# Kernel optimization log

Measured on AMD Instinct MI355X. Metric: run time of the kernel, lower is better.

Reference implementation:

```python
import jax, jax.numpy as jnp
import numpy as np

N_NODES = 100000
N_EDGES = 1600000
F_IN = 256
HID = 128
N_CLS = 64
K_APPNP = 10
ALPHA = 0.1


def setup_inputs() -> dict:
    key = jax.random.key(0)
    ks = jax.random.split(key, 12)
    x = jax.random.normal(ks[0], (N_NODES, F_IN), dtype=jnp.float32)
    edge_index = jax.random.randint(ks[1], (2, N_EDGES), 0, N_NODES, dtype=jnp.int64)
    def lin(k, fan_in, fan_out):
        s = 1.0 / np.sqrt(fan_in)
        kw, kb = jax.random.split(k)
        W = jax.random.uniform(kw, (fan_in, fan_out), minval=-s, maxval=s, dtype=jnp.float32)
        b = jax.random.uniform(kb, (fan_out,), minval=-s, maxval=s, dtype=jnp.float32)
        return W, b
    W1, b1 = lin(ks[2], F_IN, HID)
    W2, b2 = lin(ks[3], HID, HID)
    Wc, bc = lin(ks[4], HID, N_CLS)
    We, be = lin(ks[5], N_CLS, N_CLS)
    return {"x": x, "edge_index": edge_index, "W1": W1, "b1": b1, "W2": W2,
            "b2": b2, "Wc": Wc, "bc": bc, "We": We, "be": be}


def reference(x, edge_index, W1, b1, W2, b2, Wc, bc, We, be):
    N = x.shape[0]
    loop = jnp.arange(N)
    row = jnp.concatenate([edge_index[0], loop])  # source nodes (+ self loops)
    col = jnp.concatenate([edge_index[1], loop])  # target nodes (+ self loops)
    # symmetric GCN normalization: deg computed on targets
    deg = jax.ops.segment_sum(jnp.ones_like(col, dtype=x.dtype), col, num_segments=N)
    dinv = jnp.where(deg > 0, jax.lax.rsqrt(deg), 0.0)
    norm = dinv[row] * dinv[col]  # [E+N]

    def prop(h):  # normalized scatter-add aggregation
        return jax.ops.segment_sum(h[row] * norm[:, None], col, num_segments=N)

    # GCNConv: transform -> propagate -> bias (dropout is eval no-op)
    h = jax.nn.relu(prop(x @ W1) + b1)
    h = jax.nn.relu(prop(h @ W2) + b2)
    logits = h @ Wc + bc
    ev = jax.nn.relu(logits @ We + be)
    # APPNP: z_{k+1} = (1-alpha) * A_hat z_k + alpha * ev
    z = ev
    for _ in range(K_APPNP):
        z = (1.0 - ALPHA) * prop(z) + ALPHA * ev
    return jax.nn.log_softmax(z, axis=1)
```

## Files before the change

### kernel.cpp

```cpp
#include <hip/hip_runtime.h>
#include <hip/hip_fp16.h>


struct __align__(16) half8 { __half2 h[4]; };
typedef _Float16 f16x8 __attribute__((ext_vector_type(8)));
typedef float f32x4 __attribute__((ext_vector_type(4)));

__global__ __launch_bounds__(256) void k_init(int* deg, int N) {
    int i = blockIdx.x * 256 + threadIdx.x;
    if (i < N) deg[i] = 1;
}

__global__ __launch_bounds__(256) void k_count(const int* __restrict__ dst,
                                               int* deg, int* __restrict__ rank, int E) {
    int e = blockIdx.x * 256 + threadIdx.x;
    if (e < E) {
        int r = atomicAdd(&deg[dst[e]], 1);
        rank[e] = r - 1;
    }
}

__global__ __launch_bounds__(256) void k_scanA(const int* __restrict__ deg, int* bs, int N) {
    __shared__ int s[256];
    int t = threadIdx.x;
    int i = blockIdx.x * 256 + t;
    int c = (i < N) ? (deg[i] - 1) : 0;
    s[t] = c; __syncthreads();
    for (int o = 128; o > 0; o >>= 1) {
        if (t < o) s[t] += s[t + o];
        __syncthreads();
    }
    if (t == 0) bs[blockIdx.x] = s[0];
}

__global__ __launch_bounds__(512) void k_scanB(int* bs, int NB) {
    __shared__ int s[512];
    int t = threadIdx.x;
    int v = (t < NB) ? bs[t] : 0;
    s[t] = v; __syncthreads();
    for (int o = 1; o < 512; o <<= 1) {
        int u = (t >= o) ? s[t - o] : 0;
        __syncthreads();
        s[t] += u;
        __syncthreads();
    }
    if (t < NB) bs[t] = s[t] - v;
}

__global__ __launch_bounds__(256) void k_scanC(const int* __restrict__ deg, const int* __restrict__ bs,
                                               int* row_ptr, float* dinv, int N) {
    __shared__ int s[256];
    int t = threadIdx.x;
    int i = blockIdx.x * 256 + t;
    int c = (i < N) ? (deg[i] - 1) : 0;
    s[t] = c; __syncthreads();
    for (int o = 1; o < 256; o <<= 1) {
        int u = (t >= o) ? s[t - o] : 0;
        __syncthreads();
        s[t] += u;
        __syncthreads();
    }
    if (i < N) {
        int off = bs[blockIdx.x];
        row_ptr[i] = off + s[t] - c;
        dinv[i] = rsqrtf((float)deg[i]);
        if (i == N - 1) row_ptr[N] = off + s[t];
    }
}

__global__ __launch_bounds__(256) void k_fill(const int* __restrict__ src, const int* __restrict__ dst,
                                              const int* __restrict__ row_ptr,
                                              const int* __restrict__ rank,
                                              int* __restrict__ csr_src, int E) {
    int e = blockIdx.x * 256 + threadIdx.x;
    if (e < E) csr_src[row_ptr[dst[e]] + rank[e]] = src[e];
}

__global__ __launch_bounds__(256) void k_fuseW(const float* __restrict__ Wc,
                                               const float* __restrict__ bc,
                                               const float* __restrict__ We,
                                               const float* __restrict__ be,
                                               float* __restrict__ Wf,
                                               float* __restrict__ bf) {
    __shared__ float sWe[64 * 64];
    int tid = threadIdx.x;
    for (int i = tid; i < 64 * 64 / 4; i += 256)
        ((float4*)sWe)[i] = ((const float4*)We)[i];
    __syncthreads();
    for (int idx = tid; idx < 128 * 64; idx += 256) {
        int r = idx >> 6, c = idx & 63;
        float s = 0.f;
#pragma unroll 8
        for (int j = 0; j < 64; j++) s += Wc[r * 64 + j] * sWe[j * 64 + c];
        Wf[idx] = s;
    }
    if (tid < 64) {
        float s = be[tid];
#pragma unroll 8
        for (int j = 0; j < 64; j++) s += bc[j] * sWe[j * 64 + tid];
        bf[tid] = s;
    }
}

__global__ __launch_bounds__(256) void k_prepW(const float* __restrict__ W,
                                               __half* __restrict__ Wt, int K) {
    int idx = blockIdx.x * 256 + threadIdx.x;
    if (idx < 128 * K) {
        int n = idx / K, k = idx % K;
        Wt[idx] = __float2half(W[k * 128 + n]);
    }
}

template <int K, bool IN_F16>
__global__ __launch_bounds__(256) void k_mfma_gemm(const void* __restrict__ Xv,
                                                   const __half* __restrict__ Wt,
                                                   const float* __restrict__ dinv,
                                                   __half* __restrict__ Y, int N) {
    constexpr int PAD = 8;
    constexpr int LDK = K + PAD;
    __shared__ __half sA[32 * LDK];
    int tid = threadIdx.x;
    int rowBase = blockIdx.x * 32;

    if (IN_F16) {
        constexpr int IT = 32 * (K / 8) / 256;
        half8 t[IT];
#pragma unroll
        for (int i = 0; i < IT; i++) {
            int idx = tid + i * 256;
            int r = idx / (K / 8), c8 = idx % (K / 8);
            int rg = rowBase + r; if (rg > N - 1) rg = N - 1;
            t[i] = *(const half8*)&((const __half*)Xv)[(long)rg * K + 8 * c8];
        }
#pragma unroll
        for (int i = 0; i < IT; i++) {
            int idx = tid + i * 256;
            int r = idx / (K / 8), c8 = idx % (K / 8);
            *(half8*)&sA[r * LDK + 8 * c8] = t[i];
        }
    } else {
        constexpr int IT = 32 * (K / 4) / 256;
        float4 t[IT];
#pragma unroll
        for (int i = 0; i < IT; i++) {
            int idx = tid + i * 256;
            int r = idx / (K / 4), c4 = idx % (K / 4);
            int rg = rowBase + r; if (rg > N - 1) rg = N - 1;
            t[i] = *(const float4*)&((const float*)Xv)[(long)rg * K + 4 * c4];
        }
#pragma unroll
        for (int i = 0; i < IT; i++) {
            int idx = tid + i * 256;
            int r = idx / (K / 4), c4 = idx % (K / 4);
            __half2* dst = (__half2*)&sA[r * LDK + 4 * c4];
            dst[0] = __floats2half2_rn(t[i].x, t[i].y);
            dst[1] = __floats2half2_rn(t[i].z, t[i].w);
        }
    }
    __syncthreads();

    int wave = tid >> 6, lane = tid & 63;
    int m = lane & 15, quad = lane >> 4;
    int rw = (wave & 1) * 16;
    int cb = (wave >> 1) * 64;

    f32x4 d[4];
#pragma unroll
    for (int ct = 0; ct < 4; ct++) d[ct] = {0.f, 0.f, 0.f, 0.f};

#pragma unroll
    for (int kh = 0; kh < K / 128; kh++) {
        f16x8 bfr[4][4];
#pragma unroll
        for (int kc = 0; kc < 4; kc++)
#pragma unroll
            for (int ct = 0; ct < 4; ct++)
                bfr[kc][ct] = *(const f16x8*)&Wt[(long)(cb + ct * 16 + m) * K + kh * 128 + kc * 32 + quad * 8];
#pragma unroll
        for (int kc = 0; kc < 4; kc++) {
            const f16x8 a = *(const f16x8*)&sA[(rw + m) * LDK + kh * 128 + kc * 32 + quad * 8];
#pragma unroll
            for (int ct = 0; ct < 4; ct++)
                d[ct] = __builtin_amdgcn_mfma_f32_16x16x32_f16(a, bfr[kc][ct], d[ct], 0, 0, 0);
        }
    }

#pragma unroll
    for (int ct = 0; ct < 4; ct++) {
        int col = cb + ct * 16 + m;
#pragma unroll
        for (int reg = 0; reg < 4; reg++) {
            int row = rowBase + rw + quad * 4 + reg;
            if (row < N)
                Y[(long)row * 128 + col] = __float2half(d[ct][reg] * dinv[row]);
        }
    }
}

__global__ __launch_bounds__(256) void k_cls(const __half* __restrict__ H,
                                             const float* __restrict__ Wf,
                                             const float* __restrict__ bf,
                                             const float* __restrict__ dinv,
                                             float* __restrict__ ev,
                                             __half* __restrict__ evs, int N) {
    __shared__ __half sH[32 * 128];
    int tid = threadIdx.x;
    long rowBase = (long)blockIdx.x * 32;
    const half8* xg = (const half8*)(H + rowBase * 128);
    {
        half8 t0 = xg[tid];
        half8 t1 = xg[tid + 256];
        ((half8*)sH)[tid] = t0;
        ((half8*)sH)[tid + 256] = t1;
    }
    __syncthreads();

    int col = tid & 63;
    int r0 = (tid >> 6) * 8;
    float acc[8];
#pragma unroll
    for (int r = 0; r < 8; r++) acc[r] = 0.f;

    for (int k = 0; k < 128; k += 4) {
        float w0 = Wf[(k + 0) * 64 + col];
        float w1 = Wf[(k + 1) * 64 + col];
        float w2 = Wf[(k + 2) * 64 + col];
        float w3 = Wf[(k + 3) * 64 + col];
#pragma unroll
        for (int r = 0; r < 8; r++) {
            const __half2 h01 = *(const __half2*)&sH[(r0 + r) * 128 + k];
            const __half2 h23 = *(const __half2*)&sH[(r0 + r) * 128 + k + 2];
            float2 f01 = __half22float2(h01);
            float2 f23 = __half22float2(h23);
            acc[r] += f01.x * w0 + f01.y * w1 + f23.x * w2 + f23.y * w3;
        }
    }
    float b = bf[col];
#pragma unroll
    for (int r = 0; r < 8; r++) {
        long row = rowBase + r0 + r;
        float v = fmaxf(acc[r] + b, 0.f);
        ev[row * 64 + col] = v;
        evs[row * 64 + col] = __float2half(v * dinv[row]);
    }
}

template <int F, int MODE>
__global__ __launch_bounds__(256) void k_prop2(const __half* __restrict__ tab,
                                               const int* __restrict__ row_ptr,
                                               const int* __restrict__ csr_src,
                                               const float* __restrict__ dinv,
                                               const float* __restrict__ bias,
                                               const void* __restrict__ evx,
                                               void* __restrict__ out, int N) {
    constexpr int LPE = F / 8;
    constexpr int S = 64 / LPE;
    int wave = threadIdx.x >> 6;
    int lane = threadIdx.x & 63;
    int node = blockIdx.x * 4 + wave;
    if (node >= N) return;
    int slot = lane / LPE;
    int fl = lane % LPE;
    const int2 se = *(const int2*)&row_ptr[node];
    int s = se.x, e = se.y;

    float acc[8], accB[8];
#pragma unroll
    for (int q = 0; q < 8; q++) { acc[q] = 0.f; accB[q] = 0.f; }

    int j = s + slot;
    for (; j + S < e; j += 2 * S) {
        const half8 a = *(const half8*)&tab[(long)csr_src[j] * F + 8 * fl];
        const half8 b = *(const half8*)&tab[(long)csr_src[j + S] * F + 8 * fl];
#pragma unroll
        for (int q = 0; q < 4; q++) {
            float2 fa = __half22float2(a.h[q]);
            float2 fb = __half22float2(b.h[q]);
            acc[2 * q] += fa.x; acc[2 * q + 1] += fa.y;
            accB[2 * q] += fb.x; accB[2 * q + 1] += fb.y;
        }
    }
    if (j < e) {
        const half8 a = *(const half8*)&tab[(long)csr_src[j] * F + 8 * fl];
#pragma unroll
        for (int q = 0; q < 4; q++) {
            float2 fa = __half22float2(a.h[q]);
            acc[2 * q] += fa.x; acc[2 * q + 1] += fa.y;
        }
    }
    if (slot == 0) {
        const half8 a = *(const half8*)&tab[(long)node * F + 8 * fl];
#pragma unroll
        for (int q = 0; q < 4; q++) {
            float2 fa = __half22float2(a.h[q]);
            acc[2 * q] += fa.x; acc[2 * q + 1] += fa.y;
        }
    }
#pragma unroll
    for (int q = 0; q < 8; q++) acc[q] += accB[q];

#pragma unroll
    for (int off = LPE; off < 64; off <<= 1) {
#pragma unroll
        for (int q = 0; q < 8; q++) acc[q] += __shfl_xor(acc[q], off, 64);
    }

    if (slot == 0) {
        float di = dinv[node];
        if (MODE == 3) {
            const float4 b0 = *(const float4*)&bias[8 * fl];
            const float4 b1 = *(const float4*)&bias[8 * fl + 4];
            half8 ov;
            ov.h[0] = __floats2half2_rn(fmaxf(di * acc[0] + b0.x, 0.f),
                                        fmaxf(di * acc[1] + b0.y, 0.f));
            ov.h[1] = __floats2half2_rn(fmaxf(di * acc[2] + b0.z, 0.f),
                                        fmaxf(di * acc[3] + b0.w, 0.f));
            ov.h[2] = __floats2half2_rn(fmaxf(di * acc[4] + b1.x, 0.f),
                                        fmaxf(di * acc[5] + b1.y, 0.f));
            ov.h[3] = __floats2half2_rn(fmaxf(di * acc[6] + b1.z, 0.f),
                                        fmaxf(di * acc[7] + b1.w, 0.f));
            *(half8*)&((__half*)out)[(long)node * F + 8 * fl] = ov;
        } else if (MODE == 1) {
            float d2 = 0.9f * di * di;
            const half8 eh = *(const half8*)&((const __half*)evx)[(long)node * F + 8 * fl];
            half8 ov;
#pragma unroll
            for (int q = 0; q < 4; q++) {
                float2 ef = __half22float2(eh.h[q]);
                float vx = d2 * acc[2 * q] + 0.1f * ef.x;
                float vy = d2 * acc[2 * q + 1] + 0.1f * ef.y;
                ov.h[q] = __floats2half2_rn(vx, vy);
            }
            *(half8*)&((__half*)out)[(long)node * F + 8 * fl] = ov;
        } else {
            float d1 = 0.9f * di;
            const float* ef = (const float*)evx + (long)node * F + 8 * fl;
            const float4 e0 = *(const float4*)ef;
            const float4 e1 = *(const float4*)(ef + 4);
            float v[8];
            v[0] = d1 * acc[0] + 0.1f * e0.x;
            v[1] = d1 * acc[1] + 0.1f * e0.y;
            v[2] = d1 * acc[2] + 0.1f * e0.z;
            v[3] = d1 * acc[3] + 0.1f * e0.w;
            v[4] = d1 * acc[4] + 0.1f * e1.x;
            v[5] = d1 * acc[5] + 0.1f * e1.y;
            v[6] = d1 * acc[6] + 0.1f * e1.z;
            v[7] = d1 * acc[7] + 0.1f * e1.w;
            float m = v[0];
#pragma unroll
            for (int q = 1; q < 8; q++) m = fmaxf(m, v[q]);
#pragma unroll
            for (int off = 1; off < LPE; off <<= 1) m = fmaxf(m, __shfl_xor(m, off, 64));
            float ssum = 0.f;
#pragma unroll
            for (int q = 0; q < 8; q++) ssum += __expf(v[q] - m);
#pragma unroll
            for (int off = 1; off < LPE; off <<= 1) ssum += __shfl_xor(ssum, off, 64);
            float lse = m + __logf(ssum);
            float* o = (float*)out + (long)node * F + 8 * fl;
            float4 v0, v1;
            v0.x = v[0] - lse; v0.y = v[1] - lse; v0.z = v[2] - lse; v0.w = v[3] - lse;
            v1.x = v[4] - lse; v1.y = v[5] - lse; v1.z = v[6] - lse; v1.w = v[7] - lse;
            *(float4*)o = v0;
            *(float4*)(o + 4) = v1;
        }
    }
}

extern "C" void kernel_launch(void* const* d_in, const int* in_sizes, int n_in,
                              void* d_out, int out_size, void* d_ws, size_t ws_size,
                              hipStream_t stream) {
    const float* x  = (const float*)d_in[0];
    const int* edges = (const int*)d_in[1];
    const float* W1 = (const float*)d_in[2];
    const float* b1 = (const float*)d_in[3];
    const float* W2 = (const float*)d_in[4];
    const float* b2 = (const float*)d_in[5];
    const float* Wc = (const float*)d_in[6];
    const float* bc = (const float*)d_in[7];
    const float* We = (const float*)d_in[8];
    const float* be = (const float*)d_in[9];

    const int N = in_sizes[0] / 256;
    const int E = in_sizes[1] / 2;
    const int* esrc = edges;
    const int* edst = edges + E;

    char* ws = (char*)d_ws;
    size_t off = 0;
    auto alloc = [&](size_t bytes) -> void* {
        void* p = ws + off;
        off += (bytes + 255) & ~(size_t)255;
        return p;
    };
    int*    deg     = (int*)alloc((size_t)N * 4);
    int*    row_ptr = (int*)alloc((size_t)(N + 1) * 4);
    float*  dinv    = (float*)alloc((size_t)N * 4);
    int*    bs      = (int*)alloc(4096 * 4);
    int*    rank    = (int*)alloc((size_t)E * 4);
    int*    csr_src = (int*)alloc((size_t)E * 4);
    __half* P       = (__half*)alloc((size_t)N * 128 * 2);
    __half* Q16     = (__half*)alloc((size_t)N * 128 * 2);
    __half* zA      = (__half*)alloc((size_t)N * 64 * 2);
    __half* zB      = (__half*)alloc((size_t)N * 64 * 2);
    __half* evs     = (__half*)alloc((size_t)N * 64 * 2);
    float*  Wf      = (float*)alloc(128 * 64 * 4);
    float*  bf      = (float*)alloc(64 * 4);
    __half* W1t     = (__half*)alloc(128 * 256 * 2);
    __half* W2t     = (__half*)alloc(128 * 128 * 2);
    float*  ev      = (float*)d_out;

    const int nbN = (N + 255) / 256;
    const int nbE = (E + 255) / 256;
    const int nbP = (N + 3) / 4;
    const int nbG = (N + 31) / 32;

    k_init<<<nbN, 256, 0, stream>>>(deg, N);
    k_count<<<nbE, 256, 0, stream>>>(edst, deg, rank, E);
    k_fuseW<<<1, 256, 0, stream>>>(Wc, bc, We, be, Wf, bf);
    k_prepW<<<(128 * 256 + 255) / 256, 256, 0, stream>>>(W1, W1t, 256);
    k_prepW<<<(128 * 128 + 255) / 256, 256, 0, stream>>>(W2, W2t, 128);
    k_scanA<<<nbN, 256, 0, stream>>>(deg, bs, N);
    k_scanB<<<1, 512, 0, stream>>>(bs, nbN);
    k_scanC<<<nbN, 256, 0, stream>>>(deg, bs, row_ptr, dinv, N);
    k_fill<<<nbE, 256, 0, stream>>>(esrc, edst, row_ptr, rank, csr_src, E);

    k_mfma_gemm<256, false><<<nbG, 256, 0, stream>>>(x, W1t, dinv, P, N);
    k_prop2<128, 3><<<nbP, 256, 0, stream>>>(P, row_ptr, csr_src, dinv, b1, nullptr, Q16, N);

    k_mfma_gemm<128, true><<<nbG, 256, 0, stream>>>(Q16, W2t, dinv, P, N);
    k_prop2<128, 3><<<nbP, 256, 0, stream>>>(P, row_ptr, csr_src, dinv, b2, nullptr, Q16, N);

    k_cls<<<N / 32, 256, 0, stream>>>(Q16, Wf, bf, dinv, ev, evs, N);

    const __half* zin = evs;
    __half* zout;
    for (int it = 0; it < 9; ++it) {
        zout = (it % 2 == 0) ? zA : zB;
        k_prop2<64, 1><<<nbP, 256, 0, stream>>>(zin, row_ptr, csr_src, dinv, nullptr, evs, zout, N);
        zin = zout;
    }
    k_prop2<64, 2><<<nbP, 256, 0, stream>>>(zin, row_ptr, csr_src, dinv, nullptr, ev, (float*)d_out, N);
}
```

Before: 1.062 ms.

## Use register-direct MFMA GEMMs, MFMA classifier, and prefetch CSR indices in propagation

The dense GEMM kernel now drops its shared-memory staging and barrier. Each wave loads A and B fragments straight from global memory into registers and double-buffers them across the K loop. The classifier kernel moves from scalar FMA to MFMA, using an fp16-transposed fused weight produced by an extra prep launch. The propagation kernel software-pipelines its csr_src index loads one iteration ahead so the gathers do not wait on index fetches. Risks include less coalesced A loads without LDS, higher register pressure, and the classifier weights now being fp16 instead of fp32.

```diff
diff --git a/kernel.cpp b/kernel.cpp
--- a/kernel.cpp
+++ b/kernel.cpp
@@ -103,11 +103,11 @@
 }
 
 __global__ __launch_bounds__(256) void k_prepW(const float* __restrict__ W,
-                                               __half* __restrict__ Wt, int K) {
+                                               __half* __restrict__ Wt, int K, int NCOL) {
     int idx = blockIdx.x * 256 + threadIdx.x;
-    if (idx < 128 * K) {
+    if (idx < NCOL * K) {
         int n = idx / K, k = idx % K;
-        Wt[idx] = __float2half(W[k * 128 + n]);
+        Wt[idx] = __float2half(W[k * NCOL + n]);
     }
 }
 
@@ -116,81 +116,72 @@
                                                    const __half* __restrict__ Wt,
                                                    const float* __restrict__ dinv,
                                                    __half* __restrict__ Y, int N) {
-    constexpr int PAD = 8;
-    constexpr int LDK = K + PAD;
-    __shared__ __half sA[32 * LDK];
-    int tid = threadIdx.x;
-    int rowBase = blockIdx.x * 32;
-
-    if (IN_F16) {
-        constexpr int IT = 32 * (K / 8) / 256;
-        half8 t[IT];
-#pragma unroll
-        for (int i = 0; i < IT; i++) {
-            int idx = tid + i * 256;
-            int r = idx / (K / 8), c8 = idx % (K / 8);
-            int rg = rowBase + r; if (rg > N - 1) rg = N - 1;
-            t[i] = *(const half8*)&((const __half*)Xv)[(long)rg * K + 8 * c8];
-        }
-#pragma unroll
-        for (int i = 0; i < IT; i++) {
-            int idx = tid + i * 256;
-            int r = idx / (K / 8), c8 = idx % (K / 8);
-            *(half8*)&sA[r * LDK + 8 * c8] = t[i];
-        }
+    constexpr int NK = K / 32;
+    const int tid = threadIdx.x;
+    const int wave = tid >> 6, lane = tid & 63;
+    const int m = lane & 15, quad = lane >> 4;
+    const int rw = (wave & 1) * 16;
+    const int cb = (wave >> 1) * 64;
+    const int rowBase = blockIdx.x * 32;
+    int rowA = rowBase + rw + m;
+    if (rowA > N - 1) rowA = N - 1;
+
+    const float*  xf = (const float*)Xv;
+    const __half* xh = (const __half*)Xv;
+    const long aOff = (long)rowA * K + quad * 8;
+
+    f32x4 d[4];
+#pragma unroll
+    for (int ct = 0; ct < 4; ++ct) d[ct] = {0.f, 0.f, 0.f, 0.f};
+
+    f16x8 a[2];
+    float4 t0[2], t1[2];
+    f16x8 b[2][4];
+
+    if constexpr (IN_F16) {
+        a[0] = *(const f16x8*)&xh[aOff];
     } else {
-        constexpr int IT = 32 * (K / 4) / 256;
-        float4 t[IT];
-#pragma unroll
-        for (int i = 0; i < IT; i++) {
-            int idx = tid + i * 256;
-            int r = idx / (K / 4), c4 = idx % (K / 4);
-            int rg = rowBase + r; if (rg > N - 1) rg = N - 1;
-            t[i] = *(const float4*)&((const float*)Xv)[(long)rg * K + 4 * c4];
-        }
-#pragma unroll
-        for (int i = 0; i < IT; i++) {
-            int idx = tid + i * 256;
-            int r = idx / (K / 4), c4 = idx % (K / 4);
-            __half2* dst = (__half2*)&sA[r * LDK + 4 * c4];
-            dst[0] = __floats2half2_rn(t[i].x, t[i].y);
-            dst[1] = __floats2half2_rn(t[i].z, t[i].w);
-        }
-    }
-    __syncthreads();
-
-    int wave = tid >> 6, lane = tid & 63;
-    int m = lane & 15, quad = lane >> 4;
-    int rw = (wave & 1) * 16;
-    int cb = (wave >> 1) * 64;
-
-    f32x4 d[4];
-#pragma unroll
-    for (int ct = 0; ct < 4; ct++) d[ct] = {0.f, 0.f, 0.f, 0.f};
-
-#pragma unroll
-    for (int kh = 0; kh < K / 128; kh++) {
-        f16x8 bfr[4][4];
-#pragma unroll
-        for (int kc = 0; kc < 4; kc++)
-#pragma unroll
-            for (int ct = 0; ct < 4; ct++)
-                bfr[kc][ct] = *(const f16x8*)&Wt[(long)(cb + ct * 16 + m) * K + kh * 128 + kc * 32 + quad * 8];
-#pragma unroll
-        for (int kc = 0; kc < 4; kc++) {
-            const f16x8 a = *(const f16x8*)&sA[(rw + m) * LDK + kh * 128 + kc * 32 + quad * 8];
-#pragma unroll
-            for (int ct = 0; ct < 4; ct++)
-                d[ct] = __builtin_amdgcn_mfma_f32_16x16x32_f16(a, bfr[kc][ct], d[ct], 0, 0, 0);
-        }
-    }
-
-#pragma unroll
-    for (int ct = 0; ct < 4; ct++) {
-        int col = cb + ct * 16 + m;
-#pragma unroll
-        for (int reg = 0; reg < 4; reg++) {
-            int row = rowBase + rw + quad * 4 + reg;
+        t0[0] = *(const float4*)&xf[aOff];
+        t1[0] = *(const float4*)&xf[aOff + 4];
+    }
+#pragma unroll
+    for (int ct = 0; ct < 4; ++ct)
+        b[0][ct] = *(const f16x8*)&Wt[(long)(cb + ct * 16 + m) * K + quad * 8];
+
+#pragma unroll
+    for (int kc = 0; kc < NK; ++kc) {
+        const int cur = kc & 1, nxt = cur ^ 1;
+        if (kc + 1 < NK) {
+            const int k1 = (kc + 1) * 32;
+            if constexpr (IN_F16) {
+                a[nxt] = *(const f16x8*)&xh[aOff + k1];
+            } else {
+                t0[nxt] = *(const float4*)&xf[aOff + k1];
+                t1[nxt] = *(const float4*)&xf[aOff + k1 + 4];
+            }
+#pragma unroll
+            for (int ct = 0; ct < 4; ++ct)
+                b[nxt][ct] = *(const f16x8*)&Wt[(long)(cb + ct * 16 + m) * K + k1 + quad * 8];
+        }
+        if constexpr (!IN_F16) {
+            f16x8 av;
+            av[0] = (_Float16)t0[cur].x; av[1] = (_Float16)t0[cur].y;
+            av[2] = (_Float16)t0[cur].z; av[3] = (_Float16)t0[cur].w;
+            av[4] = (_Float16)t1[cur].x; av[5] = (_Float16)t1[cur].y;
+            av[6] = (_Float16)t1[cur].z; av[7] = (_Float16)t1[cur].w;
+            a[cur] = av;
+        }
+#pragma unroll
+        for (int ct = 0; ct < 4; ++ct)
+            d[ct] = __builtin_amdgcn_mfma_f32_16x16x32_f16(a[cur], b[cur][ct], d[ct], 0, 0, 0);
+    }
+
+#pragma unroll
+    for (int ct = 0; ct < 4; ++ct) {
+        const int col = cb + ct * 16 + m;
+#pragma unroll
+        for (int reg = 0; reg < 4; ++reg) {
+            const int row = rowBase + rw + quad * 4 + reg;
             if (row < N)
                 Y[(long)row * 128 + col] = __float2half(d[ct][reg] * dinv[row]);
         }
@@ -198,50 +189,56 @@
 }
 
 __global__ __launch_bounds__(256) void k_cls(const __half* __restrict__ H,
-                                             const float* __restrict__ Wf,
+                                             const __half* __restrict__ Wft,
                                              const float* __restrict__ bf,
                                              const float* __restrict__ dinv,
                                              float* __restrict__ ev,
                                              __half* __restrict__ evs, int N) {
-    __shared__ __half sH[32 * 128];
-    int tid = threadIdx.x;
-    long rowBase = (long)blockIdx.x * 32;
-    const half8* xg = (const half8*)(H + rowBase * 128);
-    {
-        half8 t0 = xg[tid];
-        half8 t1 = xg[tid + 256];
-        ((half8*)sH)[tid] = t0;
-        ((half8*)sH)[tid + 256] = t1;
-    }
-    __syncthreads();
-
-    int col = tid & 63;
-    int r0 = (tid >> 6) * 8;
-    float acc[8];
-#pragma unroll
-    for (int r = 0; r < 8; r++) acc[r] = 0.f;
-
-    for (int k = 0; k < 128; k += 4) {
-        float w0 = Wf[(k + 0) * 64 + col];
-        float w1 = Wf[(k + 1) * 64 + col];
-        float w2 = Wf[(k + 2) * 64 + col];
-        float w3 = Wf[(k + 3) * 64 + col];
-#pragma unroll
-        for (int r = 0; r < 8; r++) {
-            const __half2 h01 = *(const __half2*)&sH[(r0 + r) * 128 + k];
-            const __half2 h23 = *(const __half2*)&sH[(r0 + r) * 128 + k + 2];
-            float2 f01 = __half22float2(h01);
-            float2 f23 = __half22float2(h23);
-            acc[r] += f01.x * w0 + f01.y * w1 + f23.x * w2 + f23.y * w3;
-        }
-    }
-    float b = bf[col];
-#pragma unroll
-    for (int r = 0; r < 8; r++) {
-        long row = rowBase + r0 + r;
-        float v = fmaxf(acc[r] + b, 0.f);
-        ev[row * 64 + col] = v;
-        evs[row * 64 + col] = __float2half(v * dinv[row]);
+    const int tid = threadIdx.x;
+    const int wave = tid >> 6, lane = tid & 63;
+    const int m = lane & 15, quad = lane >> 4;
+    const int rowT = blockIdx.x * 64 + wave * 16;
+    int rowA = rowT + m;
+    if (rowA > N - 1) rowA = N - 1;
+    const long aOff = (long)rowA * 128 + quad * 8;
+
+    f32x4 d[4];
+#pragma unroll
+    for (int ct = 0; ct < 4; ++ct) d[ct] = {0.f, 0.f, 0.f, 0.f};
+
+    f16x8 a[2], b[2][4];
+    a[0] = *(const f16x8*)&H[aOff];
+#pragma unroll
+    for (int ct = 0; ct < 4; ++ct)
+        b[0][ct] = *(const f16x8*)&Wft[(long)(ct * 16 + m) * 128 + quad * 8];
+
+#pragma unroll
+    for (int kc = 0; kc < 4; ++kc) {
+        const int cur = kc & 1, nxt = cur ^ 1;
+        if (kc + 1 < 4) {
+            const int k1 = (kc + 1) * 32;
+            a[nxt] = *(const f16x8*)&H[aOff + k1];
+#pragma unroll
+            for (int ct = 0; ct < 4; ++ct)
+                b[nxt][ct] = *(const f16x8*)&Wft[(long)(ct * 16 + m) * 128 + k1 + quad * 8];
+        }
+#pragma unroll
+        for (int ct = 0; ct < 4; ++ct)
+            d[ct] = __builtin_amdgcn_mfma_f32_16x16x32_f16(a[cur], b[cur][ct], d[ct], 0, 0, 0);
+    }
+
+#pragma unroll
+    for (int ct = 0; ct < 4; ++ct) {
+        const int col = ct * 16 + m;
+#pragma unroll
+        for (int reg = 0; reg < 4; ++reg) {
+            const int row = rowT + quad * 4 + reg;
+            if (row < N) {
+                float v = fmaxf(d[ct][reg] + bf[col], 0.f);
+                ev[(long)row * 64 + col] = v;
+                evs[(long)row * 64 + col] = __float2half(v * dinv[row]);
+            }
+        }
     }
 }
 
@@ -269,9 +266,16 @@
     for (int q = 0; q < 8; q++) { acc[q] = 0.f; accB[q] = 0.f; }
 
     int j = s + slot;
-    for (; j + S < e; j += 2 * S) {
-        const half8 a = *(const half8*)&tab[(long)csr_src[j] * F + 8 * fl];
-        const half8 b = *(const half8*)&tab[(long)csr_src[j + S] * F + 8 * fl];
+    int i0 = 0, i1 = 0;
+    if (j < e) i0 = csr_src[j];
+    if (j + S < e) i1 = csr_src[j + S];
+    while (j + S < e) {
+        const int jn = j + 2 * S;
+        int n0 = 0, n1 = 0;
+        if (jn < e) n0 = csr_src[jn];
+        if (jn + S < e) n1 = csr_src[jn + S];
+        const half8 a = *(const half8*)&tab[(long)i0 * F + 8 * fl];
+        const half8 b = *(const half8*)&tab[(long)i1 * F + 8 * fl];
 #pragma unroll
         for (int q = 0; q < 4; q++) {
             float2 fa = __half22float2(a.h[q]);
@@ -279,9 +283,10 @@
             acc[2 * q] += fa.x; acc[2 * q + 1] += fa.y;
             accB[2 * q] += fb.x; accB[2 * q + 1] += fb.y;
         }
+        i0 = n0; i1 = n1; j = jn;
     }
     if (j < e) {
-        const half8 a = *(const half8*)&tab[(long)csr_src[j] * F + 8 * fl];
+        const half8 a = *(const half8*)&tab[(long)i0 * F + 8 * fl];
 #pragma unroll
         for (int q = 0; q < 4; q++) {
             float2 fa = __half22float2(a.h[q]);
@@ -408,18 +413,21 @@
     float*  bf      = (float*)alloc(64 * 4);
     __half* W1t     = (__half*)alloc(128 * 256 * 2);
     __half* W2t     = (__half*)alloc(128 * 128 * 2);
+    __half* Wft     = (__half*)alloc(64 * 128 * 2);
     float*  ev      = (float*)d_out;
 
     const int nbN = (N + 255) / 256;
     const int nbE = (E + 255) / 256;
     const int nbP = (N + 3) / 4;
     const int nbG = (N + 31) / 32;
+    const int nbC = (N + 63) / 64;
 
     k_init<<<nbN, 256, 0, stream>>>(deg, N);
     k_count<<<nbE, 256, 0, stream>>>(edst, deg, rank, E);
     k_fuseW<<<1, 256, 0, stream>>>(Wc, bc, We, be, Wf, bf);
-    k_prepW<<<(128 * 256 + 255) / 256, 256, 0, stream>>>(W1, W1t, 256);
-    k_prepW<<<(128 * 128 + 255) / 256, 256, 0, stream>>>(W2, W2t, 128);
+    k_prepW<<<(128 * 256 + 255) / 256, 256, 0, stream>>>(W1, W1t, 256, 128);
+    k_prepW<<<(128 * 128 + 255) / 256, 256, 0, stream>>>(W2, W2t, 128, 128);
+    k_prepW<<<(64 * 128 + 255) / 256, 256, 0, stream>>>(Wf, Wft, 128, 64);
     k_scanA<<<nbN, 256, 0, stream>>>(deg, bs, N);
     k_scanB<<<1, 512, 0, stream>>>(bs, nbN);
     k_scanC<<<nbN, 256, 0, stream>>>(deg, bs, row_ptr, dinv, N);
@@ -431,7 +439,7 @@
     k_mfma_gemm<128, true><<<nbG, 256, 0, stream>>>(Q16, W2t, dinv, P, N);
     k_prop2<128, 3><<<nbP, 256, 0, stream>>>(P, row_ptr, csr_src, dinv, b2, nullptr, Q16, N);
 
-    k_cls<<<N / 32, 256, 0, stream>>>(Q16, Wf, bf, dinv, ev, evs, N);
+    k_cls<<<nbC, 256, 0, stream>>>(Q16, Wft, bf, dinv, ev, evs, N);
 
     const __half* zin = evs;
     __half* zout;
```

Measured after the change: 1.030 ms. 3.0% less time.
